# Performance work log

Hardware: AMD Instinct MI355X
Metric: run time of the kernel (lower is better)

Reference implementation:

```python
import jax, jax.numpy as jnp
import numpy as np

STAGE_NUM = 5
BETA = 1.0
EPS = 1e-6


def _em_refine(cls, proto):
    # cls: [b, d]; proto: [k, d]. Matches torch einsum('bd,bkd->bk') with
    # batch-replicated prototypes == cls @ proto.T (no (b,k,d) materialization).
    p = proto
    for _ in range(STAGE_NUM):
        r = jax.nn.softmax(cls @ p.T, axis=1)          # [b, k]
        p = r.T @ cls                                   # [k, d]
        p = p / (jnp.linalg.norm(p, axis=1, keepdims=True) + EPS)
    return p


def setup_inputs() -> dict:
    key = jax.random.key(0)
    k1, k2 = jax.random.split(key)
    b, d, k = 8192, 1024, 512
    cls = jax.random.normal(k1, (b, d), dtype=jnp.float32)
    proto = jax.random.normal(k2, (k, d), dtype=jnp.float32)
    # __init__ normalizes prototypes to unit norm (with 1e-6 in denominator)
    proto = proto / (1e-6 + jnp.linalg.norm(proto, axis=1, keepdims=True))
    return {"cls": cls, "prototypes": proto}


def reference(cls, prototypes):
    # EM loop runs under torch.no_grad() -> stop_gradient here.
    new_proto = jax.lax.stop_gradient(_em_refine(cls, prototypes))  # [k, d]
    dot = cls @ new_proto.T                                          # [b, k]
    r = jax.nn.softmax(dot, axis=1)
    z_recon = r @ new_proto                                          # [b, d]
    z_out = BETA * z_recon + cls
    return (r, z_out)
```

## Files before the change

### kernel.cpp

```cpp
#include <hip/hip_runtime.h>

typedef short v8s __attribute__((ext_vector_type(8)));
typedef _Float16 v8h __attribute__((ext_vector_type(8)));
typedef float v4f __attribute__((ext_vector_type(4)));

typedef __attribute__((address_space(1))) const void* as1_void_cp;
typedef __attribute__((address_space(3))) void* as3_void_p;

__device__ __forceinline__ unsigned short f2bf(float x) {
  union { float f; unsigned int u; } v; v.f = x;
  unsigned int r = v.u + 0x7fffu + ((v.u >> 16) & 1u);
  return (unsigned short)(r >> 16);
}
__device__ __forceinline__ float bf2f(unsigned short h) {
  union { unsigned int u; float f; } v; v.u = ((unsigned int)h) << 16;
  return v.f;
}
__device__ __forceinline__ unsigned short f2h(float x) {
  _Float16 h = (_Float16)x;
  return __builtin_bit_cast(unsigned short, h);
}

template <bool ADD>
__global__ __launch_bounds__(256) void gemm_f16(
    const unsigned short* __restrict__ A, const unsigned short* __restrict__ B,
    float* __restrict__ C, const float* __restrict__ Cadd,
    int N, int lda, int ldb, int klen, size_t csplit) {
  __shared__ __align__(16) unsigned short As[128 * 128];
  __shared__ __align__(16) unsigned short Bs[128 * 128];
  const int tid = threadIdx.x;
  const int bn = blockIdx.x * 128, bm = blockIdx.y * 128;
  const int k0 = blockIdx.z * klen;
  float* Cp = C + (size_t)blockIdx.z * csplit;

  const unsigned short* ag0 = A + (size_t)(bm + (tid >> 2)) * lda + ((tid & 3) << 3) + k0;
  const unsigned short* ag1 = ag0 + (size_t)64 * lda;
  const unsigned short* bg0 = B + (size_t)(bn + (tid >> 2)) * ldb + ((tid & 3) << 3) + k0;
  const unsigned short* bg1 = bg0 + (size_t)64 * ldb;

  const int lane = tid & 63;
  const int q = lane >> 4, m15 = lane & 15;
  const int w = tid >> 6;
  const int wr = (w >> 1) * 64, wc = (w & 1) * 64;

  v4f acc[4][4];
#pragma unroll
  for (int i = 0; i < 4; ++i)
#pragma unroll
    for (int j = 0; j < 4; ++j) acc[i][j] = 0.f;

  for (int kk = 0; kk < klen; kk += 128) {
#pragma unroll
    for (int h = 0; h < 4; ++h) {
      __builtin_amdgcn_global_load_lds((as1_void_cp)(ag0 + kk + 32 * h),
                                       (as3_void_p)(As + h * 4096 + tid * 8), 16, 0, 0);
      __builtin_amdgcn_global_load_lds((as1_void_cp)(ag1 + kk + 32 * h),
                                       (as3_void_p)(As + h * 4096 + 2048 + tid * 8), 16, 0, 0);
      __builtin_amdgcn_global_load_lds((as1_void_cp)(bg0 + kk + 32 * h),
                                       (as3_void_p)(Bs + h * 4096 + tid * 8), 16, 0, 0);
      __builtin_amdgcn_global_load_lds((as1_void_cp)(bg1 + kk + 32 * h),
                                       (as3_void_p)(Bs + h * 4096 + 2048 + tid * 8), 16, 0, 0);
    }
    __syncthreads();
#pragma unroll
    for (int h = 0; h < 4; ++h) {
      v8s af[4], bf[4];
#pragma unroll
      for (int i = 0; i < 4; ++i)
        af[i] = *(const v8s*)(As + h * 4096 + (wr + i * 16 + m15) * 32 + q * 8);
#pragma unroll
      for (int j = 0; j < 4; ++j)
        bf[j] = *(const v8s*)(Bs + h * 4096 + (wc + j * 16 + m15) * 32 + q * 8);
#pragma unroll
      for (int i = 0; i < 4; ++i)
#pragma unroll
        for (int j = 0; j < 4; ++j)
          acc[i][j] = __builtin_amdgcn_mfma_f32_16x16x32_f16(
              __builtin_bit_cast(v8h, af[i]), __builtin_bit_cast(v8h, bf[j]), acc[i][j], 0, 0, 0);
    }
    __syncthreads();
  }

#pragma unroll
  for (int i = 0; i < 4; ++i) {
#pragma unroll
    for (int j = 0; j < 4; ++j) {
      const int col = bn + wc + j * 16 + m15;
#pragma unroll
      for (int rr = 0; rr < 4; ++rr) {
        const int row = bm + wr + i * 16 + q * 4 + rr;
        const size_t idx = (size_t)row * N + col;
        float v = acc[i][j][rr];
        if (ADD) v += Cadd[idx];
        Cp[idx] = v;
      }
    }
  }
}

__global__ __launch_bounds__(256) void gemm_bt3(
    const unsigned short* __restrict__ Ah, const unsigned short* __restrict__ Al,
    const unsigned short* __restrict__ Bh, const unsigned short* __restrict__ Bl,
    float* __restrict__ C, int N, int lda, int ldb, int klen, size_t csplit) {
  __shared__ __align__(16) unsigned short Ash[128 * 32];
  __shared__ __align__(16) unsigned short Asl[128 * 32];
  __shared__ __align__(16) unsigned short Bsh[128 * 32];
  __shared__ __align__(16) unsigned short Bsl[128 * 32];
  const int tid = threadIdx.x;
  const int bn = blockIdx.x * 128, bm = blockIdx.y * 128;
  const int k0 = blockIdx.z * klen;
  float* Cp = C + (size_t)blockIdx.z * csplit;

  const size_t aoff = (size_t)(bm + (tid >> 2)) * lda + ((tid & 3) << 3) + k0;
  const size_t boff = (size_t)(bn + (tid >> 2)) * ldb + ((tid & 3) << 3) + k0;
  const unsigned short* agh0 = Ah + aoff;
  const unsigned short* agh1 = agh0 + (size_t)64 * lda;
  const unsigned short* agl0 = Al + aoff;
  const unsigned short* agl1 = agl0 + (size_t)64 * lda;
  const unsigned short* bgh0 = Bh + boff;
  const unsigned short* bgh1 = bgh0 + (size_t)64 * ldb;
  const unsigned short* bgl0 = Bl + boff;
  const unsigned short* bgl1 = bgl0 + (size_t)64 * ldb;

  const int lane = tid & 63;
  const int q = lane >> 4, m15 = lane & 15;
  const int w = tid >> 6;
  const int wr = (w >> 1) * 64, wc = (w & 1) * 64;

  v4f acc[4][4];
#pragma unroll
  for (int i = 0; i < 4; ++i)
#pragma unroll
    for (int j = 0; j < 4; ++j) acc[i][j] = 0.f;

  for (int kk = 0; kk < klen; kk += 32) {
    __builtin_amdgcn_global_load_lds((as1_void_cp)(agh0 + kk), (as3_void_p)(Ash + tid * 8), 16, 0, 0);
    __builtin_amdgcn_global_load_lds((as1_void_cp)(agh1 + kk), (as3_void_p)(Ash + 2048 + tid * 8), 16, 0, 0);
    __builtin_amdgcn_global_load_lds((as1_void_cp)(agl0 + kk), (as3_void_p)(Asl + tid * 8), 16, 0, 0);
    __builtin_amdgcn_global_load_lds((as1_void_cp)(agl1 + kk), (as3_void_p)(Asl + 2048 + tid * 8), 16, 0, 0);
    __builtin_amdgcn_global_load_lds((as1_void_cp)(bgh0 + kk), (as3_void_p)(Bsh + tid * 8), 16, 0, 0);
    __builtin_amdgcn_global_load_lds((as1_void_cp)(bgh1 + kk), (as3_void_p)(Bsh + 2048 + tid * 8), 16, 0, 0);
    __builtin_amdgcn_global_load_lds((as1_void_cp)(bgl0 + kk), (as3_void_p)(Bsl + tid * 8), 16, 0, 0);
    __builtin_amdgcn_global_load_lds((as1_void_cp)(bgl1 + kk), (as3_void_p)(Bsl + 2048 + tid * 8), 16, 0, 0);
    __syncthreads();
    v8s afh[4], afl[4], bfh[4], bfl[4];
#pragma unroll
    for (int i = 0; i < 4; ++i) {
      const int ro = (wr + i * 16 + m15) * 32 + q * 8;
      afh[i] = *(const v8s*)(Ash + ro);
      afl[i] = *(const v8s*)(Asl + ro);
    }
#pragma unroll
    for (int j = 0; j < 4; ++j) {
      const int ro = (wc + j * 16 + m15) * 32 + q * 8;
      bfh[j] = *(const v8s*)(Bsh + ro);
      bfl[j] = *(const v8s*)(Bsl + ro);
    }
#pragma unroll
    for (int i = 0; i < 4; ++i)
#pragma unroll
      for (int j = 0; j < 4; ++j) {
        acc[i][j] = __builtin_amdgcn_mfma_f32_16x16x32_bf16(afh[i], bfh[j], acc[i][j], 0, 0, 0);
        acc[i][j] = __builtin_amdgcn_mfma_f32_16x16x32_bf16(afh[i], bfl[j], acc[i][j], 0, 0, 0);
        acc[i][j] = __builtin_amdgcn_mfma_f32_16x16x32_bf16(afl[i], bfh[j], acc[i][j], 0, 0, 0);
      }
    __syncthreads();
  }

#pragma unroll
  for (int i = 0; i < 4; ++i) {
#pragma unroll
    for (int j = 0; j < 4; ++j) {
      const int col = bn + wc + j * 16 + m15;
#pragma unroll
      for (int rr = 0; rr < 4; ++rr) {
        const int row = bm + wr + i * 16 + q * 4 + rr;
        Cp[(size_t)row * N + col] = acc[i][j][rr];
      }
    }
  }
}

__global__ __launch_bounds__(256) void cast_split_transpose_cls(
    const float* __restrict__ cls,
    unsigned short* __restrict__ ch, unsigned short* __restrict__ cl,
    unsigned short* __restrict__ cTh, unsigned short* __restrict__ cTl) {
  __shared__ unsigned short th[64][72];
  __shared__ unsigned short tl[64][72];
  const int d0 = blockIdx.x * 64, b0 = blockIdx.y * 64;
  const int t = threadIdx.x;
#pragma unroll
  for (int i = 0; i < 4; ++i) {
    int flat = t + i * 256;
    int bl_ = flat >> 4;
    int dl = (flat & 15) << 2;
    float4 v = *(const float4*)(cls + (size_t)(b0 + bl_) * 1024 + d0 + dl);
    ushort4 h, l;
    h.x = f2bf(v.x); l.x = f2bf(v.x - bf2f(h.x));
    h.y = f2bf(v.y); l.y = f2bf(v.y - bf2f(h.y));
    h.z = f2bf(v.z); l.z = f2bf(v.z - bf2f(h.z));
    h.w = f2bf(v.w); l.w = f2bf(v.w - bf2f(h.w));
    *(ushort4*)(ch + (size_t)(b0 + bl_) * 1024 + d0 + dl) = h;
    *(ushort4*)(cl + (size_t)(b0 + bl_) * 1024 + d0 + dl) = l;
    th[bl_][dl] = h.x; th[bl_][dl + 1] = h.y; th[bl_][dl + 2] = h.z; th[bl_][dl + 3] = h.w;
    tl[bl_][dl] = l.x; tl[bl_][dl + 1] = l.y; tl[bl_][dl + 2] = l.z; tl[bl_][dl + 3] = l.w;
  }
  __syncthreads();
#pragma unroll
  for (int i = 0; i < 4; ++i) {
    int flat = t + i * 256;
    int dl = flat >> 4;
    int bl_ = (flat & 15) << 2;
    ushort4 h = make_ushort4(th[bl_][dl], th[bl_ + 1][dl], th[bl_ + 2][dl], th[bl_ + 3][dl]);
    ushort4 l = make_ushort4(tl[bl_][dl], tl[bl_ + 1][dl], tl[bl_ + 2][dl], tl[bl_ + 3][dl]);
    *(ushort4*)(cTh + (size_t)(d0 + dl) * 8192 + b0 + bl_) = h;
    *(ushort4*)(cTl + (size_t)(d0 + dl) * 8192 + b0 + bl_) = l;
  }
}

__global__ __launch_bounds__(256) void split_f32(const float* __restrict__ in,
                                                 unsigned short* __restrict__ hi,
                                                 unsigned short* __restrict__ lo) {
  const size_t i = (size_t)(blockIdx.x * blockDim.x + threadIdx.x) * 4;
  float4 v = *(const float4*)(in + i);
  ushort4 h, l;
  h.x = f2bf(v.x); l.x = f2bf(v.x - bf2f(h.x));
  h.y = f2bf(v.y); l.y = f2bf(v.y - bf2f(h.y));
  h.z = f2bf(v.z); l.z = f2bf(v.z - bf2f(h.z));
  h.w = f2bf(v.w); l.w = f2bf(v.w - bf2f(h.w));
  *(ushort4*)(hi + i) = h;
  *(ushort4*)(lo + i) = l;
}

__global__ __launch_bounds__(256) void fuse_to_f16_dual(
    const unsigned short* __restrict__ h0, const unsigned short* __restrict__ l0,
    unsigned short* __restrict__ o0,
    const unsigned short* __restrict__ h1, const unsigned short* __restrict__ l1,
    unsigned short* __restrict__ o1) {
  const int half = blockIdx.x >> 12;
  const unsigned short* hi = half ? h1 : h0;
  const unsigned short* lo = half ? l1 : l0;
  unsigned short* out = half ? o1 : o0;
  const size_t i = ((size_t)(blockIdx.x & 4095) * 256 + threadIdx.x) * 8;
  ushort4 ha = *(const ushort4*)(hi + i);
  ushort4 hb = *(const ushort4*)(hi + i + 4);
  ushort4 la = *(const ushort4*)(lo + i);
  ushort4 lb = *(const ushort4*)(lo + i + 4);
  ushort4 oa, ob;
  oa.x = f2h(bf2f(ha.x) + bf2f(la.x)); oa.y = f2h(bf2f(ha.y) + bf2f(la.y));
  oa.z = f2h(bf2f(ha.z) + bf2f(la.z)); oa.w = f2h(bf2f(ha.w) + bf2f(la.w));
  ob.x = f2h(bf2f(hb.x) + bf2f(lb.x)); ob.y = f2h(bf2f(hb.y) + bf2f(lb.y));
  ob.z = f2h(bf2f(hb.z) + bf2f(lb.z)); ob.w = f2h(bf2f(hb.w) + bf2f(lb.w));
  *(ushort4*)(out + i) = oa;
  *(ushort4*)(out + i + 4) = ob;
}

template <bool HILO>
__global__ __launch_bounds__(512) void rowsoftmax_T(
    const float* __restrict__ SP0, const float* __restrict__ SP1,
    unsigned short* __restrict__ rTh, unsigned short* __restrict__ rTl) {
  __shared__ __align__(16) unsigned short th[32 * 520];
  __shared__ __align__(16) unsigned short tl[HILO ? 32 * 520 : 8];
  const int t = threadIdx.x;
  const int lane = t & 63, w = t >> 6;
  const int b0 = blockIdx.x * 32;
#pragma unroll
  for (int k = 0; k < 4; ++k) {
    const int bl = w * 4 + k;
    const int row = b0 + bl;
    const size_t off = (size_t)row * 512 + lane * 8;
    float4 v0 = *(const float4*)(SP0 + off);
    float4 v1 = *(const float4*)(SP0 + off + 4);
    float4 u0 = *(const float4*)(SP1 + off);
    float4 u1 = *(const float4*)(SP1 + off + 4);
    float e[8];
    e[0] = v0.x + u0.x; e[1] = v0.y + u0.y; e[2] = v0.z + u0.z; e[3] = v0.w + u0.w;
    e[4] = v1.x + u1.x; e[5] = v1.y + u1.y; e[6] = v1.z + u1.z; e[7] = v1.w + u1.w;
    float m = fmaxf(fmaxf(fmaxf(e[0], e[1]), fmaxf(e[2], e[3])),
                    fmaxf(fmaxf(e[4], e[5]), fmaxf(e[6], e[7])));
    for (int o = 32; o; o >>= 1) m = fmaxf(m, __shfl_xor(m, o));
    float s = 0.f;
#pragma unroll
    for (int i = 0; i < 8; ++i) { e[i] = __expf(e[i] - m); s += e[i]; }
    for (int o = 32; o; o >>= 1) s += __shfl_xor(s, o);
    const float inv = 1.f / s;
    unsigned short ph[8], pl[8];
#pragma unroll
    for (int i = 0; i < 8; ++i) {
      const float r = e[i] * inv;
      if constexpr (HILO) {
        ph[i] = f2bf(r);
        pl[i] = f2bf(r - bf2f(ph[i]));
      } else {
        ph[i] = f2h(r);
      }
    }
    *(v8s*)&th[bl * 520 + lane * 8] = *(v8s*)ph;
    if constexpr (HILO) *(v8s*)&tl[bl * 520 + lane * 8] = *(v8s*)pl;
  }
  __syncthreads();
  const int c = t;
  unsigned short uh[32];
#pragma unroll
  for (int b = 0; b < 32; ++b) uh[b] = th[b * 520 + c];
#pragma unroll
  for (int q = 0; q < 4; ++q)
    *(v8s*)(rTh + (size_t)c * 8192 + b0 + q * 8) = *(v8s*)&uh[q * 8];
  if constexpr (HILO) {
    unsigned short ul[32];
#pragma unroll
    for (int b = 0; b < 32; ++b) ul[b] = tl[b * 520 + c];
#pragma unroll
    for (int q = 0; q < 4; ++q)
      *(v8s*)(rTl + (size_t)c * 8192 + b0 + q * 8) = *(v8s*)&ul[q * 8];
  }
}

__global__ __launch_bounds__(256) void softmax_rows(const float* __restrict__ SP0,
                                                    const float* __restrict__ SP1,
                                                    float* __restrict__ r_out,
                                                    unsigned short* __restrict__ r_g) {
  const int w = threadIdx.x >> 6, lane = threadIdx.x & 63;
  const int row = blockIdx.x * 4 + w;
  const size_t off = (size_t)row * 512 + lane * 8;
  float4 v0 = *(const float4*)(SP0 + off);
  float4 v1 = *(const float4*)(SP0 + off + 4);
  float4 u0 = *(const float4*)(SP1 + off);
  float4 u1 = *(const float4*)(SP1 + off + 4);
  v0.x += u0.x; v0.y += u0.y; v0.z += u0.z; v0.w += u0.w;
  v1.x += u1.x; v1.y += u1.y; v1.z += u1.z; v1.w += u1.w;
  float m = fmaxf(fmaxf(fmaxf(v0.x, v0.y), fmaxf(v0.z, v0.w)),
                  fmaxf(fmaxf(v1.x, v1.y), fmaxf(v1.z, v1.w)));
  for (int off2 = 32; off2; off2 >>= 1) m = fmaxf(m, __shfl_xor(m, off2));
  float e0 = __expf(v0.x - m), e1 = __expf(v0.y - m), e2 = __expf(v0.z - m), e3 = __expf(v0.w - m);
  float e4 = __expf(v1.x - m), e5 = __expf(v1.y - m), e6 = __expf(v1.z - m), e7 = __expf(v1.w - m);
  float s = e0 + e1 + e2 + e3 + e4 + e5 + e6 + e7;
  for (int off2 = 32; off2; off2 >>= 1) s += __shfl_xor(s, off2);
  const float inv = 1.f / s;
  e0 *= inv; e1 *= inv; e2 *= inv; e3 *= inv; e4 *= inv; e5 *= inv; e6 *= inv; e7 *= inv;
  float* rp = r_out + off;
  *(float4*)rp = make_float4(e0, e1, e2, e3);
  *(float4*)(rp + 4) = make_float4(e4, e5, e6, e7);
  unsigned short* bp = r_g + off;
  *(ushort4*)bp = make_ushort4(f2h(e0), f2h(e1), f2h(e2), f2h(e3));
  *(ushort4*)(bp + 4) = make_ushort4(f2h(e4), f2h(e5), f2h(e6), f2h(e7));
}

__global__ __launch_bounds__(256) void reduce_normalize(const float* __restrict__ Pp,
                                                        unsigned short* __restrict__ pg,
                                                        unsigned short* __restrict__ pTg) {
  __shared__ float red[4];
  const int c = blockIdx.x, t = threadIdx.x;
  float ax = 0.f, ay = 0.f, az = 0.f, aw = 0.f;
#pragma unroll
  for (int s = 0; s < 16; ++s) {
    const float4 v = *(const float4*)(Pp + ((size_t)s * 512 + c) * 1024 + t * 4);
    ax += v.x; ay += v.y; az += v.z; aw += v.w;
  }
  float ss = ax * ax + ay * ay + az * az + aw * aw;
  for (int off = 32; off; off >>= 1) ss += __shfl_xor(ss, off);
  const int w = t >> 6, lane = t & 63;
  if (!lane) red[w] = ss;
  __syncthreads();
  const float tot = red[0] + red[1] + red[2] + red[3];
  const float scale = 1.f / (sqrtf(tot) + 1e-6f);
  ax *= scale; ay *= scale; az *= scale; aw *= scale;
  *(ushort4*)(pg + (size_t)c * 1024 + t * 4) =
      make_ushort4(f2h(ax), f2h(ay), f2h(az), f2h(aw));
  pTg[(size_t)(t * 4 + 0) * 512 + c] = f2h(ax);
  pTg[(size_t)(t * 4 + 1) * 512 + c] = f2h(ay);
  pTg[(size_t)(t * 4 + 2) * 512 + c] = f2h(az);
  pTg[(size_t)(t * 4 + 3) * 512 + c] = f2h(aw);
}

extern "C" void kernel_launch(void* const* d_in, const int* in_sizes, int n_in,
                              void* d_out, int out_size, void* d_ws, size_t ws_size,
                              hipStream_t stream) {
  const float* cls = (const float*)d_in[0];
  const float* proto = (const float*)d_in[1];
  float* out_r = (float*)d_out;
  float* out_z = out_r + (size_t)8192 * 512;

  char* w = (char*)d_ws;
  unsigned short* cls_h = (unsigned short*)w; w += (size_t)8192 * 1024 * 2;
  unsigned short* cls_l = (unsigned short*)w; w += (size_t)8192 * 1024 * 2;
  unsigned short* clsT_h = (unsigned short*)w; w += (size_t)1024 * 8192 * 2;
  unsigned short* clsT_l = (unsigned short*)w; w += (size_t)1024 * 8192 * 2;
  unsigned short* p_h = (unsigned short*)w; w += (size_t)512 * 1024 * 2;
  unsigned short* p_l = (unsigned short*)w; w += (size_t)512 * 1024 * 2;
  unsigned short* p_g = (unsigned short*)w; w += (size_t)512 * 1024 * 2;
  unsigned short* pT_g = (unsigned short*)w; w += (size_t)1024 * 512 * 2;
  unsigned short* rT_h = (unsigned short*)w; w += (size_t)512 * 8192 * 2;
  unsigned short* rT_l = (unsigned short*)w; w += (size_t)512 * 8192 * 2;
  float* SP = (float*)w;
  float* SP1 = SP + (size_t)8192 * 512;
  unsigned short* cls_g = cls_l;
  unsigned short* clsT_g = clsT_l;

  cast_split_transpose_cls<<<dim3(16, 128), 256, 0, stream>>>(cls, cls_h, cls_l, clsT_h, clsT_l);
  split_f32<<<512, 256, 0, stream>>>(proto, p_h, p_l);

  gemm_bt3<<<dim3(4, 64, 2), 256, 0, stream>>>(cls_h, cls_l, p_h, p_l, SP,
                                               512, 1024, 1024, 512,
                                               (size_t)8192 * 512);
  rowsoftmax_T<true><<<256, 512, 0, stream>>>(SP, SP1, rT_h, rT_l);
  gemm_bt3<<<dim3(8, 4, 16), 256, 0, stream>>>(rT_h, rT_l, clsT_h, clsT_l, SP,
                                               1024, 8192, 8192, 512,
                                               (size_t)512 * 1024);
  fuse_to_f16_dual<<<8192, 256, 0, stream>>>(cls_h, cls_l, cls_g, clsT_h, clsT_l, clsT_g);
  reduce_normalize<<<512, 256, 0, stream>>>(SP, p_g, pT_g);

  for (int it = 0; it < 4; ++it) {
    gemm_f16<false><<<dim3(4, 64, 2), 256, 0, stream>>>(cls_g, p_g, SP, nullptr,
                                                        512, 1024, 1024, 512,
                                                        (size_t)8192 * 512);
    rowsoftmax_T<false><<<256, 512, 0, stream>>>(SP, SP1, rT_h, nullptr);
    gemm_f16<false><<<dim3(8, 4, 16), 256, 0, stream>>>(rT_h, clsT_g, SP, nullptr,
                                                        1024, 8192, 8192, 512,
                                                        (size_t)512 * 1024);
    reduce_normalize<<<512, 256, 0, stream>>>(SP, p_g, pT_g);
  }

  gemm_f16<false><<<dim3(4, 64, 2), 256, 0, stream>>>(cls_g, p_g, SP, nullptr,
                                                      512, 1024, 1024, 512,
                                                      (size_t)8192 * 512);
  softmax_rows<<<2048, 256, 0, stream>>>(SP, SP1, out_r, rT_h);
  gemm_f16<true><<<dim3(8, 64, 1), 256, 0, stream>>>(rT_h, pT_g, out_z, cls,
                                                     1024, 512, 512, 512, 0);
}
```

Baseline: 502.1 us.

## Add 64x128 f16 GEMM tile, drop split-K for score GEMMs

Adds a 64x128-tile f16 GEMM kernel with a 64-wide K step and uses it for the refinement-loop GEMMs. The score GEMM no longer uses split-K, so the softmax kernels read a single partial instead of summing two. The prototype-update GEMM goes from 16 to 8 K-splits, and the reduce step takes the split count as a parameter. The existing 128x128 kernel also shrinks its K step from 128 to 64 to cut LDS use. The aim is better occupancy and fewer partial-sum reads, at the cost of lower per-block data reuse.

```diff
diff --git a/kernel.cpp b/kernel.cpp
--- a/kernel.cpp
+++ b/kernel.cpp
@@ -26,8 +26,8 @@
     const unsigned short* __restrict__ A, const unsigned short* __restrict__ B,
     float* __restrict__ C, const float* __restrict__ Cadd,
     int N, int lda, int ldb, int klen, size_t csplit) {
-  __shared__ __align__(16) unsigned short As[128 * 128];
-  __shared__ __align__(16) unsigned short Bs[128 * 128];
+  __shared__ __align__(16) unsigned short As[128 * 64];
+  __shared__ __align__(16) unsigned short Bs[128 * 64];
   const int tid = threadIdx.x;
   const int bn = blockIdx.x * 128, bm = blockIdx.y * 128;
   const int k0 = blockIdx.z * klen;
@@ -49,9 +49,9 @@
 #pragma unroll
     for (int j = 0; j < 4; ++j) acc[i][j] = 0.f;
 
-  for (int kk = 0; kk < klen; kk += 128) {
-#pragma unroll
-    for (int h = 0; h < 4; ++h) {
+  for (int kk = 0; kk < klen; kk += 64) {
+#pragma unroll
+    for (int h = 0; h < 2; ++h) {
       __builtin_amdgcn_global_load_lds((as1_void_cp)(ag0 + kk + 32 * h),
                                        (as3_void_p)(As + h * 4096 + tid * 8), 16, 0, 0);
       __builtin_amdgcn_global_load_lds((as1_void_cp)(ag1 + kk + 32 * h),
@@ -63,7 +63,7 @@
     }
     __syncthreads();
 #pragma unroll
-    for (int h = 0; h < 4; ++h) {
+    for (int h = 0; h < 2; ++h) {
       v8s af[4], bf[4];
 #pragma unroll
       for (int i = 0; i < 4; ++i)
@@ -93,6 +93,75 @@
         float v = acc[i][j][rr];
         if (ADD) v += Cadd[idx];
         Cp[idx] = v;
+      }
+    }
+  }
+}
+
+__global__ __launch_bounds__(256) void gemm_f16_64x128(
+    const unsigned short* __restrict__ A, const unsigned short* __restrict__ B,
+    float* __restrict__ C, int N, int lda, int ldb, int klen, size_t csplit) {
+  __shared__ __align__(16) unsigned short As[2 * 64 * 32];
+  __shared__ __align__(16) unsigned short Bs[2 * 128 * 32];
+  const int tid = threadIdx.x;
+  const int bn = blockIdx.x * 128, bm = blockIdx.y * 64;
+  const int k0 = blockIdx.z * klen;
+  float* Cp = C + (size_t)blockIdx.z * csplit;
+
+  const unsigned short* ag0 = A + (size_t)(bm + (tid >> 2)) * lda + ((tid & 3) << 3) + k0;
+  const unsigned short* bg0 = B + (size_t)(bn + (tid >> 2)) * ldb + ((tid & 3) << 3) + k0;
+  const unsigned short* bg1 = bg0 + (size_t)64 * ldb;
+
+  const int lane = tid & 63;
+  const int q = lane >> 4, m15 = lane & 15;
+  const int w = tid >> 6;
+  const int wc = w * 32;
+
+  v4f acc[4][2];
+#pragma unroll
+  for (int i = 0; i < 4; ++i)
+#pragma unroll
+    for (int j = 0; j < 2; ++j) acc[i][j] = 0.f;
+
+  for (int kk = 0; kk < klen; kk += 64) {
+#pragma unroll
+    for (int h = 0; h < 2; ++h) {
+      __builtin_amdgcn_global_load_lds((as1_void_cp)(ag0 + kk + 32 * h),
+                                       (as3_void_p)(As + h * 2048 + tid * 8), 16, 0, 0);
+      __builtin_amdgcn_global_load_lds((as1_void_cp)(bg0 + kk + 32 * h),
+                                       (as3_void_p)(Bs + h * 4096 + tid * 8), 16, 0, 0);
+      __builtin_amdgcn_global_load_lds((as1_void_cp)(bg1 + kk + 32 * h),
+                                       (as3_void_p)(Bs + h * 4096 + 2048 + tid * 8), 16, 0, 0);
+    }
+    __syncthreads();
+#pragma unroll
+    for (int h = 0; h < 2; ++h) {
+      v8s af[4], bf[2];
+#pragma unroll
+      for (int i = 0; i < 4; ++i)
+        af[i] = *(const v8s*)(As + h * 2048 + (i * 16 + m15) * 32 + q * 8);
+#pragma unroll
+      for (int j = 0; j < 2; ++j)
+        bf[j] = *(const v8s*)(Bs + h * 4096 + (wc + j * 16 + m15) * 32 + q * 8);
+#pragma unroll
+      for (int i = 0; i < 4; ++i)
+#pragma unroll
+        for (int j = 0; j < 2; ++j)
+          acc[i][j] = __builtin_amdgcn_mfma_f32_16x16x32_f16(
+              __builtin_bit_cast(v8h, af[i]), __builtin_bit_cast(v8h, bf[j]), acc[i][j], 0, 0, 0);
+    }
+    __syncthreads();
+  }
+
+#pragma unroll
+  for (int i = 0; i < 4; ++i) {
+#pragma unroll
+    for (int j = 0; j < 2; ++j) {
+      const int col = bn + wc + j * 16 + m15;
+#pragma unroll
+      for (int rr = 0; rr < 4; ++rr) {
+        const int row = bm + i * 16 + q * 4 + rr;
+        Cp[(size_t)row * N + col] = acc[i][j][rr];
       }
     }
   }
@@ -255,7 +324,7 @@
   *(ushort4*)(out + i + 4) = ob;
 }
 
-template <bool HILO>
+template <bool HILO, bool DUAL>
 __global__ __launch_bounds__(512) void rowsoftmax_T(
     const float* __restrict__ SP0, const float* __restrict__ SP1,
     unsigned short* __restrict__ rTh, unsigned short* __restrict__ rTl) {
@@ -271,11 +340,15 @@
     const size_t off = (size_t)row * 512 + lane * 8;
     float4 v0 = *(const float4*)(SP0 + off);
     float4 v1 = *(const float4*)(SP0 + off + 4);
-    float4 u0 = *(const float4*)(SP1 + off);
-    float4 u1 = *(const float4*)(SP1 + off + 4);
     float e[8];
-    e[0] = v0.x + u0.x; e[1] = v0.y + u0.y; e[2] = v0.z + u0.z; e[3] = v0.w + u0.w;
-    e[4] = v1.x + u1.x; e[5] = v1.y + u1.y; e[6] = v1.z + u1.z; e[7] = v1.w + u1.w;
+    e[0] = v0.x; e[1] = v0.y; e[2] = v0.z; e[3] = v0.w;
+    e[4] = v1.x; e[5] = v1.y; e[6] = v1.z; e[7] = v1.w;
+    if constexpr (DUAL) {
+      float4 u0 = *(const float4*)(SP1 + off);
+      float4 u1 = *(const float4*)(SP1 + off + 4);
+      e[0] += u0.x; e[1] += u0.y; e[2] += u0.z; e[3] += u0.w;
+      e[4] += u1.x; e[5] += u1.y; e[6] += u1.z; e[7] += u1.w;
+    }
     float m = fmaxf(fmaxf(fmaxf(e[0], e[1]), fmaxf(e[2], e[3])),
                     fmaxf(fmaxf(e[4], e[5]), fmaxf(e[6], e[7])));
     for (int o = 32; o; o >>= 1) m = fmaxf(m, __shfl_xor(m, o));
@@ -316,19 +389,14 @@
   }
 }
 
-__global__ __launch_bounds__(256) void softmax_rows(const float* __restrict__ SP0,
-                                                    const float* __restrict__ SP1,
+__global__ __launch_bounds__(256) void softmax_rows(const float* __restrict__ S,
                                                     float* __restrict__ r_out,
                                                     unsigned short* __restrict__ r_g) {
   const int w = threadIdx.x >> 6, lane = threadIdx.x & 63;
   const int row = blockIdx.x * 4 + w;
   const size_t off = (size_t)row * 512 + lane * 8;
-  float4 v0 = *(const float4*)(SP0 + off);
-  float4 v1 = *(const float4*)(SP0 + off + 4);
-  float4 u0 = *(const float4*)(SP1 + off);
-  float4 u1 = *(const float4*)(SP1 + off + 4);
-  v0.x += u0.x; v0.y += u0.y; v0.z += u0.z; v0.w += u0.w;
-  v1.x += u1.x; v1.y += u1.y; v1.z += u1.z; v1.w += u1.w;
+  float4 v0 = *(const float4*)(S + off);
+  float4 v1 = *(const float4*)(S + off + 4);
   float m = fmaxf(fmaxf(fmaxf(v0.x, v0.y), fmaxf(v0.z, v0.w)),
                   fmaxf(fmaxf(v1.x, v1.y), fmaxf(v1.z, v1.w)));
   for (int off2 = 32; off2; off2 >>= 1) m = fmaxf(m, __shfl_xor(m, off2));
@@ -347,13 +415,13 @@
 }
 
 __global__ __launch_bounds__(256) void reduce_normalize(const float* __restrict__ Pp,
+                                                        int nz,
                                                         unsigned short* __restrict__ pg,
                                                         unsigned short* __restrict__ pTg) {
   __shared__ float red[4];
   const int c = blockIdx.x, t = threadIdx.x;
   float ax = 0.f, ay = 0.f, az = 0.f, aw = 0.f;
-#pragma unroll
-  for (int s = 0; s < 16; ++s) {
+  for (int s = 0; s < nz; ++s) {
     const float4 v = *(const float4*)(Pp + ((size_t)s * 512 + c) * 1024 + t * 4);
     ax += v.x; ay += v.y; az += v.z; aw += v.w;
   }
@@ -403,28 +471,26 @@
   gemm_bt3<<<dim3(4, 64, 2), 256, 0, stream>>>(cls_h, cls_l, p_h, p_l, SP,
                                                512, 1024, 1024, 512,
                                                (size_t)8192 * 512);
-  rowsoftmax_T<true><<<256, 512, 0, stream>>>(SP, SP1, rT_h, rT_l);
+  rowsoftmax_T<true, true><<<256, 512, 0, stream>>>(SP, SP1, rT_h, rT_l);
   gemm_bt3<<<dim3(8, 4, 16), 256, 0, stream>>>(rT_h, rT_l, clsT_h, clsT_l, SP,
                                                1024, 8192, 8192, 512,
                                                (size_t)512 * 1024);
   fuse_to_f16_dual<<<8192, 256, 0, stream>>>(cls_h, cls_l, cls_g, clsT_h, clsT_l, clsT_g);
-  reduce_normalize<<<512, 256, 0, stream>>>(SP, p_g, pT_g);
+  reduce_normalize<<<512, 256, 0, stream>>>(SP, 16, p_g, pT_g);
 
   for (int it = 0; it < 4; ++it) {
-    gemm_f16<false><<<dim3(4, 64, 2), 256, 0, stream>>>(cls_g, p_g, SP, nullptr,
-                                                        512, 1024, 1024, 512,
-                                                        (size_t)8192 * 512);
-    rowsoftmax_T<false><<<256, 512, 0, stream>>>(SP, SP1, rT_h, nullptr);
-    gemm_f16<false><<<dim3(8, 4, 16), 256, 0, stream>>>(rT_h, clsT_g, SP, nullptr,
-                                                        1024, 8192, 8192, 512,
-                                                        (size_t)512 * 1024);
-    reduce_normalize<<<512, 256, 0, stream>>>(SP, p_g, pT_g);
-  }
-
-  gemm_f16<false><<<dim3(4, 64, 2), 256, 0, stream>>>(cls_g, p_g, SP, nullptr,
-                                                      512, 1024, 1024, 512,
-                                                      (size_t)8192 * 512);
-  softmax_rows<<<2048, 256, 0, stream>>>(SP, SP1, out_r, rT_h);
+    gemm_f16_64x128<<<dim3(4, 128, 1), 256, 0, stream>>>(cls_g, p_g, SP,
+                                                         512, 1024, 1024, 1024, 0);
+    rowsoftmax_T<false, false><<<256, 512, 0, stream>>>(SP, nullptr, rT_h, nullptr);
+    gemm_f16_64x128<<<dim3(8, 8, 8), 256, 0, stream>>>(rT_h, clsT_g, SP,
+                                                       1024, 8192, 8192, 1024,
+                                                       (size_t)512 * 1024);
+    reduce_normalize<<<512, 256, 0, stream>>>(SP, 8, p_g, pT_g);
+  }
+
+  gemm_f16_64x128<<<dim3(4, 128, 1), 256, 0, stream>>>(cls_g, p_g, SP,
+                                                       512, 1024, 1024, 1024, 0);
+  softmax_rows<<<2048, 256, 0, stream>>>(SP, out_r, rT_h);
   gemm_f16<true><<<dim3(8, 64, 1), 256, 0, stream>>>(rT_h, pT_g, out_z, cls,
                                                      1024, 512, 512, 512, 0);
 }
```

After: 491.4 us. -2.1%, faster.
